# Performance work log

Measured on AMD Instinct MI355X. Metric: run time of the kernel, lower is better.

## Reference

```python
import jax, jax.numpy as jnp
import numpy as np

N = 8192
FIN = 128
FOUT = 128
ALPHA = 0.2  # LeakyReLU negative slope
NEG_INF = -9e15


def setup_inputs() -> dict:
    key = jax.random.key(0)
    k1, k2, k3, k4, k5 = jax.random.split(key, 5)
    v_i = jax.random.normal(k1, (N, FIN), dtype=jnp.float32)
    v_j = jax.random.normal(k2, (N, FIN), dtype=jnp.float32)
    adj = jax.random.randint(k3, (N, N), 0, 2, dtype=jnp.int32)
    # Xavier-uniform-like init for params (gain 1.414 as in source)
    gain = 1.414
    limW = gain * np.sqrt(6.0 / (FIN + FOUT))
    W = jax.random.uniform(k4, (FIN, FOUT), jnp.float32, -limW, limW)
    lima = gain * np.sqrt(6.0 / (2 * FOUT + 1))
    a = jax.random.uniform(k5, (2 * FOUT, 1), jnp.float32, -lima, lima)
    return {"v_i": v_i, "v_j": v_j, "adj": adj, "W": W, "a": a}


def reference(v_i, v_j, adj, W, a):
    # Project node features: (N, fin) @ (fin, fout) -> (N, fout)
    h_i = v_i @ W
    h_j = v_j @ W
    # GAT decomposition of concat([h_i, h_j]) @ a:
    # e_ij = leakyrelu(h_i . a[:fout] + h_j . a[fout:])
    a1 = a[:FOUT, 0]  # (fout,)
    a2 = a[FOUT:, 0]  # (fout,)
    e = jax.nn.leaky_relu(h_i @ a1[:, None] + (h_j @ a2)[None, :], ALPHA)  # (N, N)
    scores = jnp.where(adj > 0, e, jnp.float32(NEG_INF))
    attention = jax.nn.softmax(scores, axis=1)
    return attention
```

## Files before the change

### kernel.cpp

```cpp
#include <hip/hip_runtime.h>

constexpr int N_ = 8192;
constexpr int FIN_ = 128;
constexpr int FOUT_ = 128;
#define ALPHA_ 0.2f
#define NEG_INF_ -9000000000000000.0f

__global__ void compute_u_kernel(const float* __restrict__ W,
                                 const float* __restrict__ a,
                                 float* __restrict__ u) {
    const int k = threadIdx.x;
    const float* row = W + k * FOUT_;
    float s1 = 0.f, s2 = 0.f;
#pragma unroll 4
    for (int o = 0; o < FOUT_; ++o) {
        const float w = row[o];
        s1 += w * a[o];
        s2 += w * a[FOUT_ + o];
    }
    u[k]        = s1;
    u[FIN_ + k] = s2;
}

__global__ __launch_bounds__(256) void compute_st_kernel(
    const float* __restrict__ v_i, const float* __restrict__ v_j,
    const float* __restrict__ u,
    float* __restrict__ s, float* __restrict__ t) {
    const int gwid = (blockIdx.x * blockDim.x + threadIdx.x) >> 6;
    const int lane = threadIdx.x & 63;
    if (gwid >= 2 * N_) return;

    const float* v;
    const float* uu;
    float* outp;
    int row;
    if (gwid < N_) { v = v_i; uu = u;         outp = s; row = gwid; }
    else           { v = v_j; uu = u + FIN_;  outp = t; row = gwid - N_; }

    const float2 vv = ((const float2*)(v + (size_t)row * FIN_))[lane];
    const float2 uv = ((const float2*)uu)[lane];
    float acc = vv.x * uv.x + vv.y * uv.y;
#pragma unroll
    for (int o = 32; o > 0; o >>= 1) acc += __shfl_xor(acc, o, 64);
    if (lane == 0) outp[row] = acc;
}

__global__ __launch_bounds__(256) void attn_softmax_kernel(
    const int* __restrict__ adj, const float* __restrict__ s,
    const float* __restrict__ t, float* __restrict__ out) {
    const int row = blockIdx.x;
    const int tid = threadIdx.x;
    const float si = s[row];

    const int4*   adj4 = (const int4*)(adj + (size_t)row * N_);
    const float4* t4   = (const float4*)t;
    float4*       out4 = (float4*)(out + (size_t)row * N_);

    float ev[32];
    float lmax = NEG_INF_;
#pragma unroll
    for (int it = 0; it < 8; ++it) {
        const int idx = it * 256 + tid;
        const int4   av = adj4[idx];
        const float4 tv = t4[idx];
        float x0 = si + tv.x; x0 = (x0 >= 0.f) ? x0 : ALPHA_ * x0;
        float x1 = si + tv.y; x1 = (x1 >= 0.f) ? x1 : ALPHA_ * x1;
        float x2 = si + tv.z; x2 = (x2 >= 0.f) ? x2 : ALPHA_ * x2;
        float x3 = si + tv.w; x3 = (x3 >= 0.f) ? x3 : ALPHA_ * x3;
        const float e0 = (av.x > 0) ? x0 : NEG_INF_;
        const float e1 = (av.y > 0) ? x1 : NEG_INF_;
        const float e2 = (av.z > 0) ? x2 : NEG_INF_;
        const float e3 = (av.w > 0) ? x3 : NEG_INF_;
        ev[it * 4 + 0] = e0;
        ev[it * 4 + 1] = e1;
        ev[it * 4 + 2] = e2;
        ev[it * 4 + 3] = e3;
        lmax = fmaxf(lmax, fmaxf(fmaxf(e0, e1), fmaxf(e2, e3)));
    }

    __shared__ float red[4];
    const int wave = tid >> 6;
    const int lane = tid & 63;

#pragma unroll
    for (int o = 32; o > 0; o >>= 1) lmax = fmaxf(lmax, __shfl_xor(lmax, o, 64));
    if (lane == 0) red[wave] = lmax;
    __syncthreads();
    const float m = fmaxf(fmaxf(red[0], red[1]), fmaxf(red[2], red[3]));
    __syncthreads();

    float lsum = 0.f;
#pragma unroll
    for (int c = 0; c < 32; ++c) {
        const float p = __expf(ev[c] - m);
        ev[c] = p;
        lsum += p;
    }

#pragma unroll
    for (int o = 32; o > 0; o >>= 1) lsum += __shfl_xor(lsum, o, 64);
    if (lane == 0) red[wave] = lsum;
    __syncthreads();
    const float total = (red[0] + red[1]) + (red[2] + red[3]);
    const float inv = 1.0f / total;

#pragma unroll
    for (int it = 0; it < 8; ++it) {
        const int idx = it * 256 + tid;
        out4[idx] = make_float4(ev[it * 4 + 0] * inv, ev[it * 4 + 1] * inv,
                                ev[it * 4 + 2] * inv, ev[it * 4 + 3] * inv);
    }
}

extern "C" void kernel_launch(void* const* d_in, const int* in_sizes, int n_in,
                              void* d_out, int out_size, void* d_ws, size_t ws_size,
                              hipStream_t stream) {
    const float* v_i = (const float*)d_in[0];
    const float* v_j = (const float*)d_in[1];
    const int*   adj = (const int*)d_in[2];
    const float* W   = (const float*)d_in[3];
    const float* a   = (const float*)d_in[4];
    float* out = (float*)d_out;

    float* ws = (float*)d_ws;
    float* u = ws;
    float* s = ws + 256;
    float* t = ws + 256 + N_;

    compute_u_kernel<<<1, 128, 0, stream>>>(W, a, u);

    compute_st_kernel<<<(2 * N_) / 4, 256, 0, stream>>>(v_i, v_j, u, s, t);

    attn_softmax_kernel<<<N_, 256, 0, stream>>>(adj, s, t, out);
}
```

Measured before the change: 449.1 us.

## Use nontemporal adj loads/out stores, 512-thread rows, parallel u kernel

The main softmax kernel now reads the adjacency matrix with nontemporal loads and writes the output with nontemporal stores, so streaming data does not pollute the cache. The block size rises to 512 threads with 16 values per thread instead of 32. The tiny u-projection kernel is spread across 64 blocks with one wavefront per output and a shuffle reduction. The kernel is bandwidth bound at roughly 512 MB of traffic, so gains depend on the cache hints. The larger block adds a wider cross-wave reduction.

New measurement: 434.4 us. -3.3%, faster.

```diff
diff --git a/kernel.cpp b/kernel.cpp
--- a/kernel.cpp
+++ b/kernel.cpp
@@ -6,20 +6,24 @@
 #define ALPHA_ 0.2f
 #define NEG_INF_ -9000000000000000.0f
 
-__global__ void compute_u_kernel(const float* __restrict__ W,
-                                 const float* __restrict__ a,
-                                 float* __restrict__ u) {
-    const int k = threadIdx.x;
-    const float* row = W + k * FOUT_;
-    float s1 = 0.f, s2 = 0.f;
-#pragma unroll 4
-    for (int o = 0; o < FOUT_; ++o) {
-        const float w = row[o];
-        s1 += w * a[o];
-        s2 += w * a[FOUT_ + o];
-    }
-    u[k]        = s1;
-    u[FIN_ + k] = s2;
+typedef int   v4i __attribute__((ext_vector_type(4)));
+typedef float v4f __attribute__((ext_vector_type(4)));
+
+__global__ __launch_bounds__(256) void compute_u_kernel(
+    const float* __restrict__ W, const float* __restrict__ a,
+    float* __restrict__ u) {
+    const int gwid = (blockIdx.x * blockDim.x + threadIdx.x) >> 6;
+    const int lane = threadIdx.x & 63;
+    if (gwid >= 2 * FOUT_) return;
+    const int k     = gwid & (FOUT_ - 1);
+    const int which = gwid >> 7;
+
+    const float2 wv = ((const float2*)(W + (size_t)k * FOUT_))[lane];
+    const float2 av = ((const float2*)(a + which * FOUT_))[lane];
+    float acc = wv.x * av.x + wv.y * av.y;
+#pragma unroll
+    for (int o = 32; o > 0; o >>= 1) acc += __shfl_xor(acc, o, 64);
+    if (lane == 0) u[which * FIN_ + k] = acc;
 }
 
 __global__ __launch_bounds__(256) void compute_st_kernel(
@@ -45,24 +49,24 @@
     if (lane == 0) outp[row] = acc;
 }
 
-__global__ __launch_bounds__(256) void attn_softmax_kernel(
+__global__ __launch_bounds__(512) void attn_softmax_kernel(
     const int* __restrict__ adj, const float* __restrict__ s,
     const float* __restrict__ t, float* __restrict__ out) {
     const int row = blockIdx.x;
     const int tid = threadIdx.x;
     const float si = s[row];
 
-    const int4*   adj4 = (const int4*)(adj + (size_t)row * N_);
-    const float4* t4   = (const float4*)t;
-    float4*       out4 = (float4*)(out + (size_t)row * N_);
+    const v4i* adj4 = (const v4i*)(adj + (size_t)row * N_);
+    const v4f* t4   = (const v4f*)t;
+    v4f*       out4 = (v4f*)(out + (size_t)row * N_);
 
-    float ev[32];
+    float ev[16];
     float lmax = NEG_INF_;
 #pragma unroll
-    for (int it = 0; it < 8; ++it) {
-        const int idx = it * 256 + tid;
-        const int4   av = adj4[idx];
-        const float4 tv = t4[idx];
+    for (int it = 0; it < 4; ++it) {
+        const int idx = it * 512 + tid;
+        const v4i av = __builtin_nontemporal_load(adj4 + idx);
+        const v4f tv = t4[idx];
         float x0 = si + tv.x; x0 = (x0 >= 0.f) ? x0 : ALPHA_ * x0;
         float x1 = si + tv.y; x1 = (x1 >= 0.f) ? x1 : ALPHA_ * x1;
         float x2 = si + tv.z; x2 = (x2 >= 0.f) ? x2 : ALPHA_ * x2;
@@ -78,7 +82,7 @@
         lmax = fmaxf(lmax, fmaxf(fmaxf(e0, e1), fmaxf(e2, e3)));
     }
 
-    __shared__ float red[4];
+    __shared__ float red[8];
     const int wave = tid >> 6;
     const int lane = tid & 63;
 
@@ -86,12 +90,14 @@
     for (int o = 32; o > 0; o >>= 1) lmax = fmaxf(lmax, __shfl_xor(lmax, o, 64));
     if (lane == 0) red[wave] = lmax;
     __syncthreads();
-    const float m = fmaxf(fmaxf(red[0], red[1]), fmaxf(red[2], red[3]));
+    float m = red[0];
+#pragma unroll
+    for (int w = 1; w < 8; ++w) m = fmaxf(m, red[w]);
     __syncthreads();
 
     float lsum = 0.f;
 #pragma unroll
-    for (int c = 0; c < 32; ++c) {
+    for (int c = 0; c < 16; ++c) {
         const float p = __expf(ev[c] - m);
         ev[c] = p;
         lsum += p;
@@ -101,14 +107,20 @@
     for (int o = 32; o > 0; o >>= 1) lsum += __shfl_xor(lsum, o, 64);
     if (lane == 0) red[wave] = lsum;
     __syncthreads();
-    const float total = (red[0] + red[1]) + (red[2] + red[3]);
+    float total = red[0];
+#pragma unroll
+    for (int w = 1; w < 8; ++w) total += red[w];
     const float inv = 1.0f / total;
 
 #pragma unroll
-    for (int it = 0; it < 8; ++it) {
-        const int idx = it * 256 + tid;
-        out4[idx] = make_float4(ev[it * 4 + 0] * inv, ev[it * 4 + 1] * inv,
-                                ev[it * 4 + 2] * inv, ev[it * 4 + 3] * inv);
+    for (int it = 0; it < 4; ++it) {
+        const int idx = it * 512 + tid;
+        v4f o;
+        o.x = ev[it * 4 + 0] * inv;
+        o.y = ev[it * 4 + 1] * inv;
+        o.z = ev[it * 4 + 2] * inv;
+        o.w = ev[it * 4 + 3] * inv;
+        __builtin_nontemporal_store(o, out4 + idx);
     }
 }
 
@@ -127,9 +139,9 @@
     float* s = ws + 256;
     float* t = ws + 256 + N_;
 
-    compute_u_kernel<<<1, 128, 0, stream>>>(W, a, u);
+    compute_u_kernel<<<64, 256, 0, stream>>>(W, a, u);
 
     compute_st_kernel<<<(2 * N_) / 4, 256, 0, stream>>>(v_i, v_j, u, s, t);
 
-    attn_softmax_kernel<<<N_, 256, 0, stream>>>(adj, s, t, out);
+    attn_softmax_kernel<<<N_, 512, 0, stream>>>(adj, s, t, out);
 }
```
